# Optimization experiments

Hardware: AMD Instinct MI355X
Metric: run time of the kernel (lower is better)

## Reference

```python
import jax, jax.numpy as jnp
import numpy as np

N = 50000
S = 32           # n_sample
D_IN = 256
D_OUT = 128
ALPHA = 0.2      # leakyrelu negative slope


def setup_inputs() -> dict:
    key = jax.random.key(0)
    k1, k2, k3, k4 = jax.random.split(key, 4)
    x = jax.random.normal(k1, (N, D_IN), dtype=jnp.float32)
    neibs = jax.random.randint(k2, (N, S), 0, N, dtype=jnp.int64)
    # xavier_uniform with gain=1.414
    limW = 1.414 * np.sqrt(6.0 / (D_IN + D_OUT))
    W = jax.random.uniform(k3, (D_IN, D_OUT), dtype=jnp.float32, minval=-limW, maxval=limW)
    lima = 1.414 * np.sqrt(6.0 / (2 * D_OUT + 1))
    a = jax.random.uniform(k4, (2 * D_OUT, 1), dtype=jnp.float32, minval=-lima, maxval=lima)
    return {"x": x, "neibs": neibs, "W": W, "a": a}


def reference(x, neibs, W, a):
    # x: [N, D_in], neibs: [N, S] int, W: [D_in, D_out], a: [2*D_out, 1]
    xw = x @ W                                  # [N, D_out]
    xn = xw[neibs]                              # [N, S, D_out] gathered neighbor feats
    # a_input @ a == xw @ a[:D_out] + xn @ a[D_out:]  (avoid materializing concat)
    a_self = a[:D_OUT, 0]                       # [D_out]
    a_neib = a[D_OUT:, 0]                       # [D_out]
    e = (xw @ a_self)[:, None] + jnp.einsum('nsd,d->ns', xn, a_neib)  # [N, S]
    e = jnp.where(e > 0, e, ALPHA * e)          # leakyrelu
    attention = jax.nn.softmax(e, axis=1)       # [N, S]  (dropout skipped: eval mode)
    h_prime = jnp.einsum('ns,nsd->nd', attention, xn)                # [N, D_out]
    output = jnp.concatenate([xw, h_prime], axis=1)                  # concat=True
    return jax.nn.elu(output)
```

## Files before the change

kernel.cpp:

```cpp
#include <hip/hip_runtime.h>
#include <math.h>

#define N_NODES 50000
#define S_NEIB 32
#define D_IN 256
#define D_OUT 128
#define ALPHA 0.2f

typedef __attribute__((ext_vector_type(8))) short bf16x8;
typedef __attribute__((ext_vector_type(4))) float f32x4;

__device__ __forceinline__ float elu_f(float v) {
    return v > 0.f ? v : (expf(v) - 1.f);
}

__device__ __forceinline__ unsigned short f2bf(float f) {
    unsigned u = __builtin_bit_cast(unsigned, f);
    u += 0x7fffu + ((u >> 16) & 1u);
    return (unsigned short)(u >> 16);
}

__global__ __launch_bounds__(256) void gemm_score_kernel(
    const float* __restrict__ x, const float* __restrict__ W,
    const float* __restrict__ a, unsigned short* __restrict__ xwb,
    float* __restrict__ s_self, float* __restrict__ s_neib,
    float* __restrict__ out)
{
    __shared__ unsigned short xs[64 * 264];
    __shared__ float ps[2][4][64];

    const int tid  = threadIdx.x;
    const int lane = tid & 63;
    const int wave = tid >> 6;
    const int q    = lane >> 4;
    const int t    = lane & 15;
    const int colW = wave * 32;
    const int r0   = blockIdx.x * 64;

    for (int i = 0; i < 16; ++i) {
        int f4  = i * 256 + tid;
        int row = f4 >> 6;
        int c4  = (f4 & 63) << 2;
        float4 v = make_float4(0.f, 0.f, 0.f, 0.f);
        if (r0 + row < N_NODES)
            v = *(const float4*)(x + (size_t)(r0 + row) * D_IN + c4);
        ushort4 b;
        b.x = f2bf(v.x); b.y = f2bf(v.y); b.z = f2bf(v.z); b.w = f2bf(v.w);
        *(ushort4*)&xs[row * 264 + c4] = b;
    }
    __syncthreads();

    f32x4 acc[4][2];
    #pragma unroll
    for (int mt = 0; mt < 4; ++mt)
        #pragma unroll
        for (int nt = 0; nt < 2; ++nt)
            acc[mt][nt] = (f32x4){0.f, 0.f, 0.f, 0.f};

    #pragma unroll
    for (int kc = 0; kc < 8; ++kc) {
        const int k0 = kc * 32 + q * 8;
        bf16x8 afrag[4];
        #pragma unroll
        for (int mt = 0; mt < 4; ++mt)
            afrag[mt] = *(const bf16x8*)&xs[(mt * 16 + t) * 264 + k0];
        bf16x8 bfrag[2];
        #pragma unroll
        for (int nt = 0; nt < 2; ++nt) {
            const float* wp = W + (size_t)k0 * D_OUT + colW + nt * 16 + t;
            #pragma unroll
            for (int j = 0; j < 8; ++j)
                bfrag[nt][j] = (short)f2bf(wp[(size_t)j * D_OUT]);
        }
        #pragma unroll
        for (int mt = 0; mt < 4; ++mt)
            #pragma unroll
            for (int nt = 0; nt < 2; ++nt)
                acc[mt][nt] = __builtin_amdgcn_mfma_f32_16x16x32_bf16(
                    afrag[mt], bfrag[nt], acc[mt][nt], 0, 0, 0);
    }

    const float as0 = a[colW + t],         as1 = a[colW + 16 + t];
    const float an0 = a[D_OUT + colW + t], an1 = a[D_OUT + colW + 16 + t];
    #pragma unroll
    for (int mt = 0; mt < 4; ++mt) {
        #pragma unroll
        for (int r = 0; r < 4; ++r) {
            float vs = acc[mt][0][r] * as0 + acc[mt][1][r] * as1;
            float vn = acc[mt][0][r] * an0 + acc[mt][1][r] * an1;
            #pragma unroll
            for (int d = 8; d >= 1; d >>= 1) {
                vs += __shfl_xor(vs, d);
                vn += __shfl_xor(vn, d);
            }
            if (t == 0) {
                int row = mt * 16 + q * 4 + r;
                ps[0][wave][row] = vs;
                ps[1][wave][row] = vn;
            }
        }
    }
    __syncthreads();
    if (tid < 64 && r0 + tid < N_NODES) {
        s_self[r0 + tid] = ps[0][0][tid] + ps[0][1][tid] + ps[0][2][tid] + ps[0][3][tid];
        s_neib[r0 + tid] = ps[1][0][tid] + ps[1][1][tid] + ps[1][2][tid] + ps[1][3][tid];
    }

    #pragma unroll
    for (int mt = 0; mt < 4; ++mt) {
        #pragma unroll
        for (int r = 0; r < 4; ++r) {
            int g = r0 + mt * 16 + q * 4 + r;
            if (g < N_NODES) {
                #pragma unroll
                for (int nt = 0; nt < 2; ++nt) {
                    int col = colW + nt * 16 + t;
                    float v = acc[mt][nt][r];
                    xwb[(size_t)g * D_OUT + col] = f2bf(v);
                    out[(size_t)g * (2 * D_OUT) + col] = elu_f(v);
                }
            }
        }
    }
}

__global__ __launch_bounds__(256) void aggregate_kernel(
    const int* __restrict__ neibs, const unsigned short* __restrict__ xwb,
    const float* __restrict__ s_self, const float* __restrict__ s_neib,
    float* __restrict__ out)
{
    const int lane = threadIdx.x & 63;
    const int wave = threadIdx.x >> 6;
    const int n = blockIdx.x * 4 + wave;
    if (n >= N_NODES) return;

    int   idx = 0;
    float e   = -1e30f;
    if (lane < 32) {
        idx = neibs[n * S_NEIB + lane];
        e = s_self[n] + s_neib[idx];
        e = e > 0.f ? e : ALPHA * e;
    }
    float m = e;
    #pragma unroll
    for (int d = 16; d >= 1; d >>= 1) m = fmaxf(m, __shfl_xor(m, d));
    float p = (lane < 32) ? __expf(e - m) : 0.f;
    float ssum = p;
    #pragma unroll
    for (int d = 16; d >= 1; d >>= 1) ssum += __shfl_xor(ssum, d);
    float att = p / ssum;

    float accx = 0.f, accy = 0.f;
    #pragma unroll
    for (int s = 0; s < 32; ++s) {
        int   j = __shfl(idx, s);
        float w = __shfl(att, s);
        unsigned v = *(const unsigned*)(xwb + (size_t)j * D_OUT + 2 * lane);
        float lo = __builtin_bit_cast(float, v << 16);
        float hi = __builtin_bit_cast(float, v & 0xffff0000u);
        accx = fmaf(w, lo, accx);
        accy = fmaf(w, hi, accy);
    }
    float2 o;
    o.x = elu_f(accx);
    o.y = elu_f(accy);
    *(float2*)(out + (size_t)n * (2 * D_OUT) + D_OUT + 2 * lane) = o;
}

extern "C" void kernel_launch(void* const* d_in, const int* in_sizes, int n_in,
                              void* d_out, int out_size, void* d_ws, size_t ws_size,
                              hipStream_t stream) {
    const float* x     = (const float*)d_in[0];
    const int*   neibs = (const int*)  d_in[1];
    const float* W     = (const float*)d_in[2];
    const float* a     = (const float*)d_in[3];
    float* out = (float*)d_out;

    unsigned short* xwb = (unsigned short*)d_ws;
    float* s_self = (float*)(xwb + (size_t)N_NODES * D_OUT);
    float* s_neib = s_self + N_NODES;

    gemm_score_kernel<<<(N_NODES + 63) / 64, 256, 0, stream>>>(
        x, W, a, xwb, s_self, s_neib, out);
    aggregate_kernel<<<(N_NODES + 3) / 4, 256, 0, stream>>>(
        neibs, xwb, s_self, s_neib, out);
}
```

Baseline: 162.1 us.

## Pre-pack W to bf16 fragment layout; split neighbor gather across wave halves

A small pre-kernel converts W to bf16 and lays it out in MFMA B-fragment order, so each GEMM block loads each fragment with one 16-byte load instead of eight strided fp32 loads plus conversions. The aggregate kernel now has each half-wave handle alternate neighbors with 8-byte row loads covering four features per lane. The two halves are combined with a cross-half shuffle, and a launch-bounds occupancy hint is added. This adds a third launch and workspace space for the packed W.

New measurement: 163.9 us. No clear change (+1.1%).

```diff
diff --git a/kernel.cpp b/kernel.cpp
--- a/kernel.cpp
+++ b/kernel.cpp
@@ -20,8 +20,19 @@
     return (unsigned short)(u >> 16);
 }
 
+__global__ __launch_bounds__(256) void pack_w_kernel(
+    const float* __restrict__ W, unsigned short* __restrict__ Wp)
+{
+    int tid = blockIdx.x * 256 + threadIdx.x;
+    int j  = tid & 7;
+    int t  = (tid >> 3) & 15;
+    int kb = (tid >> 7) & 31;
+    int c  = tid >> 12;
+    Wp[tid] = f2bf(W[(kb * 8 + j) * D_OUT + c * 16 + t]);
+}
+
 __global__ __launch_bounds__(256) void gemm_score_kernel(
-    const float* __restrict__ x, const float* __restrict__ W,
+    const float* __restrict__ x, const unsigned short* __restrict__ Wp,
     const float* __restrict__ a, unsigned short* __restrict__ xwb,
     float* __restrict__ s_self, float* __restrict__ s_neib,
     float* __restrict__ out)
@@ -50,6 +61,8 @@
     }
     __syncthreads();
 
+    const bf16x8* Wp8 = (const bf16x8*)Wp;
+
     f32x4 acc[4][2];
     #pragma unroll
     for (int mt = 0; mt < 4; ++mt)
@@ -66,12 +79,8 @@
             afrag[mt] = *(const bf16x8*)&xs[(mt * 16 + t) * 264 + k0];
         bf16x8 bfrag[2];
         #pragma unroll
-        for (int nt = 0; nt < 2; ++nt) {
-            const float* wp = W + (size_t)k0 * D_OUT + colW + nt * 16 + t;
-            #pragma unroll
-            for (int j = 0; j < 8; ++j)
-                bfrag[nt][j] = (short)f2bf(wp[(size_t)j * D_OUT]);
-        }
+        for (int nt = 0; nt < 2; ++nt)
+            bfrag[nt] = Wp8[((wave * 2 + nt) * 32 + kc * 4 + q) * 16 + t];
         #pragma unroll
         for (int mt = 0; mt < 4; ++mt)
             #pragma unroll
@@ -124,7 +133,7 @@
     }
 }
 
-__global__ __launch_bounds__(256) void aggregate_kernel(
+__global__ __launch_bounds__(256, 4) void aggregate_kernel(
     const int* __restrict__ neibs, const unsigned short* __restrict__ xwb,
     const float* __restrict__ s_self, const float* __restrict__ s_neib,
     float* __restrict__ out)
@@ -134,6 +143,9 @@
     const int n = blockIdx.x * 4 + wave;
     if (n >= N_NODES) return;
 
+    const int half = lane >> 5;
+    const int hl   = lane & 31;
+
     int   idx = 0;
     float e   = -1e30f;
     if (lane < 32) {
@@ -150,21 +162,35 @@
     for (int d = 16; d >= 1; d >>= 1) ssum += __shfl_xor(ssum, d);
     float att = p / ssum;
 
-    float accx = 0.f, accy = 0.f;
-    #pragma unroll
-    for (int s = 0; s < 32; ++s) {
+    float a0 = 0.f, a1 = 0.f, a2 = 0.f, a3 = 0.f;
+    #pragma unroll
+    for (int s2 = 0; s2 < 16; ++s2) {
+        int   s = s2 * 2 + half;
         int   j = __shfl(idx, s);
         float w = __shfl(att, s);
-        unsigned v = *(const unsigned*)(xwb + (size_t)j * D_OUT + 2 * lane);
-        float lo = __builtin_bit_cast(float, v << 16);
-        float hi = __builtin_bit_cast(float, v & 0xffff0000u);
-        accx = fmaf(w, lo, accx);
-        accy = fmaf(w, hi, accy);
-    }
-    float2 o;
-    o.x = elu_f(accx);
-    o.y = elu_f(accy);
-    *(float2*)(out + (size_t)n * (2 * D_OUT) + D_OUT + 2 * lane) = o;
+        uint2 v = *(const uint2*)(xwb + (size_t)j * D_OUT + 4 * hl);
+        float f0 = __builtin_bit_cast(float, v.x << 16);
+        float f1 = __builtin_bit_cast(float, v.x & 0xffff0000u);
+        float f2 = __builtin_bit_cast(float, v.y << 16);
+        float f3 = __builtin_bit_cast(float, v.y & 0xffff0000u);
+        a0 = fmaf(w, f0, a0);
+        a1 = fmaf(w, f1, a1);
+        a2 = fmaf(w, f2, a2);
+        a3 = fmaf(w, f3, a3);
+    }
+    a0 += __shfl_xor(a0, 32);
+    a1 += __shfl_xor(a1, 32);
+    a2 += __shfl_xor(a2, 32);
+    a3 += __shfl_xor(a3, 32);
+
+    if (half == 0) {
+        float4 o;
+        o.x = elu_f(a0);
+        o.y = elu_f(a1);
+        o.z = elu_f(a2);
+        o.w = elu_f(a3);
+        *(float4*)(out + (size_t)n * (2 * D_OUT) + D_OUT + 4 * hl) = o;
+    }
 }
 
 extern "C" void kernel_launch(void* const* d_in, const int* in_sizes, int n_in,
@@ -179,9 +205,11 @@
     unsigned short* xwb = (unsigned short*)d_ws;
     float* s_self = (float*)(xwb + (size_t)N_NODES * D_OUT);
     float* s_neib = s_self + N_NODES;
-
+    unsigned short* Wp = (unsigned short*)(s_neib + N_NODES);
+
+    pack_w_kernel<<<128, 256, 0, stream>>>(W, Wp);
     gemm_score_kernel<<<(N_NODES + 63) / 64, 256, 0, stream>>>(
-        x, W, a, xwb, s_self, s_neib, out);
+        x, Wp, a, xwb, s_self, s_neib, out);
     aggregate_kernel<<<(N_NODES + 3) / 4, 256, 0, stream>>>(
         neibs, xwb, s_self, s_neib, out);
 }
```
